# Optimization experiments

Measured on AMD Instinct MI355X. Metric: run time of the kernel, lower is better.

## Reference

```python
import jax, jax.numpy as jnp
import numpy as np

B, L, C, H, RATIO = 2, 512, 256, 8, 4
D = C // H
EPS = 1e-5


def layernorm(x, g, b):
    m = jnp.mean(x, axis=-1, keepdims=True)
    v = jnp.mean((x - m) ** 2, axis=-1, keepdims=True)
    return (x - m) * jax.lax.rsqrt(v + EPS) * g + b


def setup_inputs() -> dict:
    key = jax.random.key(0)
    ks = jax.random.split(key, 10)
    s = 0.02
    return {
        "x": jax.random.normal(ks[0], (B, L, C), jnp.float32),
        "relative_pos": jax.random.normal(ks[1], (B, L, L, C), jnp.float32),
        # attention params (qkv_bias=False)
        "w_qkv": jax.random.normal(ks[2], (C, 3 * C), jnp.float32) * s,
        "w_proj": jax.random.normal(ks[3], (C, C), jnp.float32) * s,
        "b_proj": jnp.zeros((C,), jnp.float32),
        # relative_project: Linear(C,H) -> GELU -> LayerNorm(H)
        "w_rel": jax.random.normal(ks[4], (C, H), jnp.float32) * s,
        "b_rel": jnp.zeros((H,), jnp.float32),
        "g_reln": jnp.ones((H,), jnp.float32),
        "b_reln": jnp.zeros((H,), jnp.float32),
        # block layernorms
        "g_n1": jnp.ones((C,), jnp.float32),
        "b_n1": jnp.zeros((C,), jnp.float32),
        "g_n2": jnp.ones((C,), jnp.float32),
        "b_n2": jnp.zeros((C,), jnp.float32),
        # MLP (mlp_ratio=4, act=GELU)
        "w_mlp1": jax.random.normal(ks[5], (C, RATIO * C), jnp.float32) * s,
        "b_mlp1": jnp.zeros((RATIO * C,), jnp.float32),
        "w_mlp2": jax.random.normal(ks[6], (RATIO * C, C), jnp.float32) * s,
        "b_mlp2": jnp.zeros((C,), jnp.float32),
    }


def reference(x, relative_pos, w_qkv, w_proj, b_proj, w_rel, b_rel,
              g_reln, b_reln, g_n1, b_n1, g_n2, b_n2,
              w_mlp1, b_mlp1, w_mlp2, b_mlp2):
    # eval mode: dropout / droppath are identity
    scale = D ** -0.5

    # --- attention branch ---
    h = layernorm(x, g_n1, b_n1)                      # [B,L,C]
    qkv = (h @ w_qkv).reshape(B, L, 3, H, D)
    qkv = jnp.transpose(qkv, (2, 0, 3, 1, 4))          # [3,B,H,L,D]
    q, k, v = qkv[0], qkv[1], qkv[2]

    attn = jnp.einsum("bhid,bhjd->bhij", q, k)        # [B,H,L,L]

    # relative bias: Linear -> GELU(exact) -> LayerNorm over heads
    rel = jax.nn.gelu(relative_pos @ w_rel + b_rel, approximate=False)  # [B,L,L,H]
    rel = layernorm(rel, g_reln, b_reln)
    rel = jnp.transpose(rel, (0, 3, 1, 2))            # [B,H,L,L]

    attn = jax.nn.softmax((attn + rel) * scale, axis=-1)
    o = jnp.einsum("bhij,bhjd->bhid", attn, v)        # [B,H,L,D]
    o = jnp.transpose(o, (0, 2, 1, 3)).reshape(B, L, C)
    o = o @ w_proj + b_proj
    x = x + o

    # --- MLP branch (jump=False since out_feat==in_feat) ---
    h = layernorm(x, g_n2, b_n2)
    h = jax.nn.gelu(h @ w_mlp1 + b_mlp1, approximate=False)
    h = h @ w_mlp2 + b_mlp2
    return x + h
```

## Files before the change

### kernel.cpp

```cpp
#include <hip/hip_runtime.h>
#include <hip/hip_bf16.h>
#include <cstddef>

#define EPS_ 1e-5f
#define SCALE_ 0.1767766952966369f

typedef short bf16x8_t __attribute__((ext_vector_type(8)));
typedef float f32x4_t  __attribute__((ext_vector_type(4)));

__device__ __forceinline__ float gelu_f(float x) {
    float y = 0.7978845608028654f * (x + 0.044715f * x * x * x);
    float e = __expf(2.0f * y);
    float t = 1.0f - 2.0f * __builtin_amdgcn_rcpf(e + 1.0f);
    return 0.5f * x * (1.0f + t);
}
__device__ __forceinline__ unsigned short f2bf(float f) {
    return __builtin_bit_cast(unsigned short, __float2bfloat16(f));
}
__device__ __forceinline__ unsigned f2bf2(float a, float b) {
    unsigned lo = __builtin_bit_cast(unsigned short, __float2bfloat16(a));
    unsigned hi = __builtin_bit_cast(unsigned short, __float2bfloat16(b));
    return lo | (hi << 16);
}
__device__ __forceinline__ float bf2f(unsigned short s) {
    unsigned u = (unsigned)s << 16;
    return __builtin_bit_cast(float, u);
}

__global__ __launch_bounds__(256) void ln_kernel(const float* __restrict__ x,
                                                 const float* __restrict__ g,
                                                 const float* __restrict__ b,
                                                 unsigned short* __restrict__ out) {
    int wid = threadIdx.x >> 6, lane = threadIdx.x & 63;
    int row = blockIdx.x * 4 + wid;
    const float4 xv = *(const float4*)(x + (size_t)row * 256 + lane * 4);
    float s  = xv.x + xv.y + xv.z + xv.w;
    float sq = xv.x*xv.x + xv.y*xv.y + xv.z*xv.z + xv.w*xv.w;
#pragma unroll
    for (int m = 1; m < 64; m <<= 1) { s += __shfl_xor(s, m); sq += __shfl_xor(sq, m); }
    float mean = s * (1.0f/256.0f);
    float var  = sq * (1.0f/256.0f) - mean*mean;
    float rstd = rsqrtf(var + EPS_);
    float4 gv = *(const float4*)(g + lane*4);
    float4 bv = *(const float4*)(b + lane*4);
    uint2 o;
    o.x = f2bf2((xv.x-mean)*rstd*gv.x + bv.x, (xv.y-mean)*rstd*gv.y + bv.y);
    o.y = f2bf2((xv.z-mean)*rstd*gv.z + bv.z, (xv.w-mean)*rstd*gv.w + bv.w);
    *(uint2*)(out + (size_t)row * 256 + lane * 4) = o;
}

__global__ __launch_bounds__(256) void convw_kernel(
    const float* __restrict__ w_qkv,  unsigned short* __restrict__ wqkvT,
    const float* __restrict__ w_proj, unsigned short* __restrict__ wprojT,
    const float* __restrict__ w_mlp1, unsigned short* __restrict__ wmlp1T,
    const float* __restrict__ w_mlp2, unsigned short* __restrict__ wmlp2T) {
    __shared__ float tile[32][33];
    int bid = blockIdx.x, t = threadIdx.x;
    const float* W; unsigned short* WT; int K, N, tt;
    if (bid < 192)      { W = w_qkv;  WT = wqkvT;  K = 256;  N = 768;  tt = bid; }
    else if (bid < 256) { W = w_proj; WT = wprojT; K = 256;  N = 256;  tt = bid - 192; }
    else if (bid < 512) { W = w_mlp1; WT = wmlp1T; K = 256;  N = 1024; tt = bid - 256; }
    else                { W = w_mlp2; WT = wmlp2T; K = 1024; N = 256;  tt = bid - 512; }
    int ntn = N >> 5;
    int kt = tt / ntn, nt = tt % ntn;
    int k0 = kt * 32, n0 = nt * 32;
    {
        int kr = t >> 3, cg = (t & 7) * 4;
        float4 v = *(const float4*)(W + (size_t)(k0 + kr) * N + n0 + cg);
        tile[kr][cg+0] = v.x; tile[kr][cg+1] = v.y; tile[kr][cg+2] = v.z; tile[kr][cg+3] = v.w;
    }
    __syncthreads();
    {
        int nr = t >> 3, kg = (t & 7) * 4;
        uint2 o;
        o.x = f2bf2(tile[kg+0][nr], tile[kg+1][nr]);
        o.y = f2bf2(tile[kg+2][nr], tile[kg+3][nr]);
        *(uint2*)(WT + (size_t)(n0 + nr) * K + k0 + kg) = o;
    }
}

template<bool BIAS, bool GACT, bool RESID, bool BF16OUT, int KSPLIT>
__global__ __launch_bounds__(256) void mgemm_kernel(
    const unsigned short* __restrict__ A, const unsigned short* __restrict__ BT,
    const float* __restrict__ bias, const float* __restrict__ resid,
    void* __restrict__ Cout, int M, int N, int K) {
    __shared__ unsigned short Al[64][40];
    __shared__ unsigned short Bl[64][40];
    int t = threadIdx.x;
    int bm = blockIdx.x, bn = blockIdx.y, kz = blockIdx.z;
    int kchunk = K / KSPLIT;
    int srow = t >> 2, skk = (t & 3) * 8;
    const unsigned short* Ap = A  + (size_t)(bm*64 + srow) * K + kz*kchunk + skk;
    const unsigned short* Bp = BT + (size_t)(bn*64 + srow) * K + kz*kchunk + skk;
    int lane = t & 63, w = t >> 6, wr = w >> 1, wc = w & 1;
    int fr = lane & 15, fg = lane >> 4;
    f32x4_t a00 = {0.f,0.f,0.f,0.f}, a01 = {0.f,0.f,0.f,0.f};
    f32x4_t a10 = {0.f,0.f,0.f,0.f}, a11 = {0.f,0.f,0.f,0.f};
    for (int kk = 0; kk < kchunk; kk += 32) {
        uint4 av = *(const uint4*)(Ap + kk);
        uint4 bv = *(const uint4*)(Bp + kk);
        __syncthreads();
        *(uint4*)&Al[srow][skk] = av;
        *(uint4*)&Bl[srow][skk] = bv;
        __syncthreads();
        bf16x8_t fa0 = *(const bf16x8_t*)&Al[wr*32      + fr][fg*8];
        bf16x8_t fa1 = *(const bf16x8_t*)&Al[wr*32 + 16 + fr][fg*8];
        bf16x8_t fb0 = *(const bf16x8_t*)&Bl[wc*32      + fr][fg*8];
        bf16x8_t fb1 = *(const bf16x8_t*)&Bl[wc*32 + 16 + fr][fg*8];
        a00 = __builtin_amdgcn_mfma_f32_16x16x32_bf16(fa0, fb0, a00, 0, 0, 0);
        a01 = __builtin_amdgcn_mfma_f32_16x16x32_bf16(fa0, fb1, a01, 0, 0, 0);
        a10 = __builtin_amdgcn_mfma_f32_16x16x32_bf16(fa1, fb0, a10, 0, 0, 0);
        a11 = __builtin_amdgcn_mfma_f32_16x16x32_bf16(fa1, fb1, a11, 0, 0, 0);
    }
    float* Cf = (float*)Cout + (KSPLIT > 1 ? (size_t)kz * M * N : (size_t)0);
    unsigned short* Cb = (unsigned short*)Cout;
    auto emit = [&](f32x4_t acc, int mi, int ni) {
        int Ro = bm*64 + wr*32 + mi*16 + fg*4;
        int Co = bn*64 + wc*32 + ni*16 + fr;
        float bval = BIAS ? bias[Co] : 0.f;
#pragma unroll
        for (int e = 0; e < 4; ++e) {
            int r = Ro + e;
            float v = acc[e];
            if (BIAS)  v += bval;
            if (GACT)  v = gelu_f(v);
            if (RESID) v += resid[(size_t)r * N + Co];
            if (BF16OUT) Cb[(size_t)r * N + Co] = f2bf(v);
            else         Cf[(size_t)r * N + Co] = v;
        }
    };
    emit(a00, 0, 0); emit(a01, 0, 1); emit(a10, 1, 0); emit(a11, 1, 1);
}

__global__ __launch_bounds__(256) void qk_kernel(const float* __restrict__ qkv,
                                                 float* __restrict__ qk) {
    __shared__ float k_lds[512*32];
    int t = threadIdx.x;
    int it = blockIdx.x;
    int h  = blockIdx.y;
    int b  = blockIdx.z;
    const float* base = qkv + (size_t)b * 393216;
#pragma unroll
    for (int r = 0; r < 16; ++r) {
        int idx = r*256 + t;
        int row = idx >> 3, c4 = idx & 7;
        float4 kv = *(const float4*)(base + (size_t)row*768 + 256 + h*32 + c4*4);
        *(float4*)(k_lds + row*32 + c4*4) = kv;
    }
    __syncthreads();
    int ir = t & 31, jg = t >> 5;
    int i = it*32 + ir;
    float4 q[8];
    const float* qp = base + (size_t)i*768 + h*32;
#pragma unroll
    for (int c4 = 0; c4 < 8; ++c4) q[c4] = *(const float4*)(qp + c4*4);
    float* outp = qk + (((size_t)(b*512 + i))*8 + h)*512 + jg*64;
    for (int jj = 0; jj < 64; jj += 4) {
        float a4[4];
#pragma unroll
        for (int u = 0; u < 4; ++u) {
            const float* kp = k_lds + (size_t)(jg*64 + jj + u)*32;
            float acc = 0.f;
#pragma unroll
            for (int c4 = 0; c4 < 8; ++c4) {
                float4 kv = *(const float4*)(kp + c4*4);
                acc += q[c4].x*kv.x + q[c4].y*kv.y + q[c4].z*kv.z + q[c4].w*kv.w;
            }
            a4[u] = acc;
        }
        *(float4*)(outp + jj) = make_float4(a4[0], a4[1], a4[2], a4[3]);
    }
}

#define LGS 520
__global__ __launch_bounds__(256) void rel_softmax_kernel(
    const float* __restrict__ rp, const float* __restrict__ qk,
    const float* __restrict__ w_rel, const float* __restrict__ b_rel,
    const float* __restrict__ g_reln, const float* __restrict__ b_reln,
    unsigned short* __restrict__ attn) {
    __shared__ float lg_lds[8*LGS];
    int t = threadIdx.x;
    int bi = blockIdx.x;
    int wid = t >> 6, lane = t & 63;
    int fr = lane & 15, fg = lane >> 4;
    bool act = fr < 8;
    bf16x8_t bfrag[8];
#pragma unroll
    for (int kk = 0; kk < 8; ++kk) {
        bf16x8_t bf;
#pragma unroll
        for (int e = 0; e < 8; ++e) {
            float v = act ? w_rel[(size_t)(kk*32 + fg*8 + e)*8 + fr] : 0.f;
            bf[e] = (short)f2bf(v);
        }
        bfrag[kk] = bf;
    }
    float brel = act ? b_rel[fr]  : 0.f;
    float grn  = act ? g_reln[fr] : 1.f;
    float brn  = act ? b_reln[fr] : 0.f;
    const float* rpb = rp + (size_t)bi * 512 * 256;
#pragma unroll 1
    for (int tile = 0; tile < 8; ++tile) {
        int j0 = wid*128 + tile*16;
        const float* arow = rpb + (size_t)(j0 + fr)*256 + fg*8;
        f32x4_t acc = {0.f,0.f,0.f,0.f};
#pragma unroll
        for (int kk = 0; kk < 8; ++kk) {
            float4 x0 = *(const float4*)(arow + kk*32);
            float4 x1 = *(const float4*)(arow + kk*32 + 4);
            union { bf16x8_t v; uint4 u; } cvt;
            cvt.u.x = f2bf2(x0.x, x0.y);
            cvt.u.y = f2bf2(x0.z, x0.w);
            cvt.u.z = f2bf2(x1.x, x1.y);
            cvt.u.w = f2bf2(x1.z, x1.w);
            acc = __builtin_amdgcn_mfma_f32_16x16x32_bf16(cvt.v, bfrag[kk], acc, 0, 0, 0);
        }
#pragma unroll
        for (int r = 0; r < 4; ++r) {
            float val = acc[r] + brel;
            float gv = gelu_f(val);
            float sm = gv, sq = gv*gv;
            sm += __shfl_xor(sm, 1); sq += __shfl_xor(sq, 1);
            sm += __shfl_xor(sm, 2); sq += __shfl_xor(sq, 2);
            sm += __shfl_xor(sm, 4); sq += __shfl_xor(sq, 4);
            float mean = sm * 0.125f;
            float var  = sq * 0.125f - mean*mean;
            float reln = (gv - mean) * rsqrtf(var + EPS_) * grn + brn;
            if (act) lg_lds[fr*LGS + j0 + fg*4 + r] = reln;
        }
    }
    __syncthreads();
    {
        int h = wid*2 + (lane >> 5);
        int sub = lane & 31;
        const float* row  = lg_lds + h*LGS;
        const float* qrow = qk + ((size_t)bi*8 + h)*512;
        float v[16];
#pragma unroll
        for (int c4 = 0; c4 < 4; ++c4) {
            float4 r4 = *(const float4*)(row  + c4*128 + sub*4);
            float4 q4 = *(const float4*)(qrow + c4*128 + sub*4);
            v[c4*4+0] = (q4.x + r4.x) * SCALE_;
            v[c4*4+1] = (q4.y + r4.y) * SCALE_;
            v[c4*4+2] = (q4.z + r4.z) * SCALE_;
            v[c4*4+3] = (q4.w + r4.w) * SCALE_;
        }
        float mx = v[0];
#pragma unroll
        for (int e = 1; e < 16; ++e) mx = fmaxf(mx, v[e]);
#pragma unroll
        for (int m = 1; m < 32; m <<= 1) mx = fmaxf(mx, __shfl_xor(mx, m));
        float s = 0.f;
#pragma unroll
        for (int e = 0; e < 16; ++e) { v[e] = __expf(v[e] - mx); s += v[e]; }
#pragma unroll
        for (int m = 1; m < 32; m <<= 1) s += __shfl_xor(s, m);
        float inv = 1.0f / s;
#pragma unroll
        for (int e = 0; e < 16; ++e) v[e] *= inv;
        unsigned short* dst = attn + (size_t)bi*4096 + h*512;
#pragma unroll
        for (int c4 = 0; c4 < 4; ++c4) {
            uint2 o2;
            o2.x = f2bf2(v[c4*4+0], v[c4*4+1]);
            o2.y = f2bf2(v[c4*4+2], v[c4*4+3]);
            *(uint2*)(dst + c4*128 + sub*4) = o2;
        }
    }
}

__global__ __launch_bounds__(256) void attnv_kernel(const unsigned short* __restrict__ attn,
                                                    const float* __restrict__ qkv,
                                                    unsigned short* __restrict__ o) {
    __shared__ float a_lds[4*8*512];
    int t = threadIdx.x;
    int bi0 = blockIdx.x * 4;
    int b = bi0 >> 9;
    const ushort4* asrc = (const ushort4*)(attn + (size_t)bi0*4096);
#pragma unroll
    for (int r = 0; r < 16; ++r) {
        ushort4 s4 = asrc[r*256 + t];
        float4 f4 = make_float4(bf2f(s4.x), bf2f(s4.y), bf2f(s4.z), bf2f(s4.w));
        *(float4*)(a_lds + (size_t)(r*256 + t)*4) = f4;
    }
    __syncthreads();
    int c = t, h = c >> 5;
    const float* vcol = qkv + (size_t)b*393216 + 512 + c;
    float acc0 = 0.f, acc1 = 0.f, acc2 = 0.f, acc3 = 0.f;
    for (int j = 0; j < 512; j += 2) {
        float vv0 = vcol[(size_t)j*768];
        float vv1 = vcol[(size_t)(j+1)*768];
        acc0 += a_lds[(0*8+h)*512 + j]*vv0 + a_lds[(0*8+h)*512 + j+1]*vv1;
        acc1 += a_lds[(1*8+h)*512 + j]*vv0 + a_lds[(1*8+h)*512 + j+1]*vv1;
        acc2 += a_lds[(2*8+h)*512 + j]*vv0 + a_lds[(2*8+h)*512 + j+1]*vv1;
        acc3 += a_lds[(3*8+h)*512 + j]*vv0 + a_lds[(3*8+h)*512 + j+1]*vv1;
    }
    o[(size_t)(bi0+0)*256 + c] = f2bf(acc0);
    o[(size_t)(bi0+1)*256 + c] = f2bf(acc1);
    o[(size_t)(bi0+2)*256 + c] = f2bf(acc2);
    o[(size_t)(bi0+3)*256 + c] = f2bf(acc3);
}

__global__ __launch_bounds__(256) void combine_kernel(const float* __restrict__ part,
                                                      const float* __restrict__ bias,
                                                      const float* __restrict__ resid,
                                                      float* __restrict__ out) {
    int f = blockIdx.x * 256 + threadIdx.x;
    int e = f * 4;
    float4 r  = *(const float4*)(resid + e);
    float4 bv = *(const float4*)(bias + (e & 255));
    float4 p0 = *(const float4*)(part + e);
    float4 p1 = *(const float4*)(part + 262144 + e);
    float4 p2 = *(const float4*)(part + 524288 + e);
    float4 p3 = *(const float4*)(part + 786432 + e);
    float4 o4;
    o4.x = r.x + bv.x + p0.x + p1.x + p2.x + p3.x;
    o4.y = r.y + bv.y + p0.y + p1.y + p2.y + p3.y;
    o4.z = r.z + bv.z + p0.z + p1.z + p2.z + p3.z;
    o4.w = r.w + bv.w + p0.w + p1.w + p2.w + p3.w;
    *(float4*)(out + e) = o4;
}

extern "C" void kernel_launch(void* const* d_in, const int* in_sizes, int n_in,
                              void* d_out, int out_size, void* d_ws, size_t ws_size,
                              hipStream_t stream) {
    const float* x      = (const float*)d_in[0];
    const float* rp     = (const float*)d_in[1];
    const float* w_qkv  = (const float*)d_in[2];
    const float* w_proj = (const float*)d_in[3];
    const float* b_proj = (const float*)d_in[4];
    const float* w_rel  = (const float*)d_in[5];
    const float* b_rel  = (const float*)d_in[6];
    const float* g_reln = (const float*)d_in[7];
    const float* b_reln = (const float*)d_in[8];
    const float* g_n1   = (const float*)d_in[9];
    const float* b_n1   = (const float*)d_in[10];
    const float* g_n2   = (const float*)d_in[11];
    const float* b_n2   = (const float*)d_in[12];
    const float* w_mlp1 = (const float*)d_in[13];
    const float* b_mlp1 = (const float*)d_in[14];
    const float* w_mlp2 = (const float*)d_in[15];
    const float* b_mlp2 = (const float*)d_in[16];
    float* out = (float*)d_out;

    float* ws      = (float*)d_ws;
    float* ws_qkv  = ws;
    float* ws_qk   = ws_qkv + 786432;
    float* ws_x1   = ws_qk  + 4194304;
    float* ws_pt   = ws_x1  + 262144;
    unsigned short* ub = (unsigned short*)(ws_pt + 1048576);
    unsigned short* attnbf = ub;
    unsigned short* hbf    = attnbf + 4194304;
    unsigned short* obf    = hbf  + 262144;
    unsigned short* h2bf   = obf  + 262144;
    unsigned short* hgbf   = h2bf + 262144;
    unsigned short* wqkvT  = hgbf + 1048576;
    unsigned short* wprojT = wqkvT + 196608;
    unsigned short* wmlp1T = wprojT + 65536;
    unsigned short* wmlp2T = wmlp1T + 262144;

    convw_kernel<<<768, 256, 0, stream>>>(w_qkv, wqkvT, w_proj, wprojT,
                                          w_mlp1, wmlp1T, w_mlp2, wmlp2T);
    ln_kernel<<<256, 256, 0, stream>>>(x, g_n1, b_n1, hbf);
    mgemm_kernel<false,false,false,false,1><<<dim3(16,12,1), 256, 0, stream>>>(
        hbf, wqkvT, nullptr, nullptr, ws_qkv, 1024, 768, 256);
    qk_kernel<<<dim3(16,8,2), 256, 0, stream>>>(ws_qkv, ws_qk);
    rel_softmax_kernel<<<1024, 256, 0, stream>>>(rp, ws_qk, w_rel, b_rel, g_reln, b_reln, attnbf);
    attnv_kernel<<<256, 256, 0, stream>>>(attnbf, ws_qkv, obf);
    mgemm_kernel<true,false,true,false,1><<<dim3(16,4,1), 256, 0, stream>>>(
        obf, wprojT, b_proj, x, ws_x1, 1024, 256, 256);
    ln_kernel<<<256, 256, 0, stream>>>(ws_x1, g_n2, b_n2, h2bf);
    mgemm_kernel<true,true,false,true,1><<<dim3(16,16,1), 256, 0, stream>>>(
        h2bf, wmlp1T, b_mlp1, nullptr, hgbf, 1024, 1024, 256);
    mgemm_kernel<false,false,false,false,4><<<dim3(16,4,4), 256, 0, stream>>>(
        hgbf, wmlp2T, nullptr, nullptr, ws_pt, 1024, 256, 1024);
    combine_kernel<<<256, 256, 0, stream>>>(ws_pt, b_mlp2, ws_x1, out);
}
```

Measured before the change: 222.9 us.

## Fuse QK^T into relative-bias softmax kernel and merge LN1 into weight prep

Removes the separate fp32 qk kernel and its 16 MB intermediate buffer. The q·k logits are now computed inside rel_softmax with a bf16 MFMA, using a per-lane selected q fragment so that each head's row block is picked out, and they are added to the relative bias before writing to LDS. The first layernorm is merged into the weight-conversion kernel as extra blocks, saving one launch. The attn·V loop is also widened to float4 LDS reads. The trade-off is that q·k now runs in bf16 instead of fp32, and K is read redundantly from global memory by every row block.

```diff
diff --git a/kernel.cpp b/kernel.cpp
--- a/kernel.cpp
+++ b/kernel.cpp
@@ -27,12 +27,11 @@
     return __builtin_bit_cast(float, u);
 }
 
-__global__ __launch_bounds__(256) void ln_kernel(const float* __restrict__ x,
-                                                 const float* __restrict__ g,
-                                                 const float* __restrict__ b,
-                                                 unsigned short* __restrict__ out) {
-    int wid = threadIdx.x >> 6, lane = threadIdx.x & 63;
-    int row = blockIdx.x * 4 + wid;
+__device__ __forceinline__ void ln_row_body(const float* __restrict__ x,
+                                            const float* __restrict__ g,
+                                            const float* __restrict__ b,
+                                            unsigned short* __restrict__ out,
+                                            int row, int lane) {
     const float4 xv = *(const float4*)(x + (size_t)row * 256 + lane * 4);
     float s  = xv.x + xv.y + xv.z + xv.w;
     float sq = xv.x*xv.x + xv.y*xv.y + xv.z*xv.z + xv.w*xv.w;
@@ -49,13 +48,26 @@
     *(uint2*)(out + (size_t)row * 256 + lane * 4) = o;
 }
 
-__global__ __launch_bounds__(256) void convw_kernel(
+__global__ __launch_bounds__(256) void ln_kernel(const float* __restrict__ x,
+                                                 const float* __restrict__ g,
+                                                 const float* __restrict__ b,
+                                                 unsigned short* __restrict__ out) {
+    ln_row_body(x, g, b, out, blockIdx.x * 4 + (threadIdx.x >> 6), threadIdx.x & 63);
+}
+
+__global__ __launch_bounds__(256) void prep_kernel(
     const float* __restrict__ w_qkv,  unsigned short* __restrict__ wqkvT,
     const float* __restrict__ w_proj, unsigned short* __restrict__ wprojT,
     const float* __restrict__ w_mlp1, unsigned short* __restrict__ wmlp1T,
-    const float* __restrict__ w_mlp2, unsigned short* __restrict__ wmlp2T) {
+    const float* __restrict__ w_mlp2, unsigned short* __restrict__ wmlp2T,
+    const float* __restrict__ x, const float* __restrict__ g_n1,
+    const float* __restrict__ b_n1, unsigned short* __restrict__ hbf) {
     __shared__ float tile[32][33];
     int bid = blockIdx.x, t = threadIdx.x;
+    if (bid >= 768) {
+        ln_row_body(x, g_n1, b_n1, hbf, (bid - 768) * 4 + (t >> 6), t & 63);
+        return;
+    }
     const float* W; unsigned short* WT; int K, N, tt;
     if (bid < 192)      { W = w_qkv;  WT = wqkvT;  K = 256;  N = 768;  tt = bid; }
     else if (bid < 256) { W = w_proj; WT = wprojT; K = 256;  N = 256;  tt = bid - 192; }
@@ -132,55 +144,16 @@
     emit(a00, 0, 0); emit(a01, 0, 1); emit(a10, 1, 0); emit(a11, 1, 1);
 }
 
-__global__ __launch_bounds__(256) void qk_kernel(const float* __restrict__ qkv,
-                                                 float* __restrict__ qk) {
-    __shared__ float k_lds[512*32];
-    int t = threadIdx.x;
-    int it = blockIdx.x;
-    int h  = blockIdx.y;
-    int b  = blockIdx.z;
-    const float* base = qkv + (size_t)b * 393216;
-#pragma unroll
-    for (int r = 0; r < 16; ++r) {
-        int idx = r*256 + t;
-        int row = idx >> 3, c4 = idx & 7;
-        float4 kv = *(const float4*)(base + (size_t)row*768 + 256 + h*32 + c4*4);
-        *(float4*)(k_lds + row*32 + c4*4) = kv;
-    }
-    __syncthreads();
-    int ir = t & 31, jg = t >> 5;
-    int i = it*32 + ir;
-    float4 q[8];
-    const float* qp = base + (size_t)i*768 + h*32;
-#pragma unroll
-    for (int c4 = 0; c4 < 8; ++c4) q[c4] = *(const float4*)(qp + c4*4);
-    float* outp = qk + (((size_t)(b*512 + i))*8 + h)*512 + jg*64;
-    for (int jj = 0; jj < 64; jj += 4) {
-        float a4[4];
-#pragma unroll
-        for (int u = 0; u < 4; ++u) {
-            const float* kp = k_lds + (size_t)(jg*64 + jj + u)*32;
-            float acc = 0.f;
-#pragma unroll
-            for (int c4 = 0; c4 < 8; ++c4) {
-                float4 kv = *(const float4*)(kp + c4*4);
-                acc += q[c4].x*kv.x + q[c4].y*kv.y + q[c4].z*kv.z + q[c4].w*kv.w;
-            }
-            a4[u] = acc;
-        }
-        *(float4*)(outp + jj) = make_float4(a4[0], a4[1], a4[2], a4[3]);
-    }
-}
-
 #define LGS 520
 __global__ __launch_bounds__(256) void rel_softmax_kernel(
-    const float* __restrict__ rp, const float* __restrict__ qk,
+    const float* __restrict__ rp, const float* __restrict__ qkv,
     const float* __restrict__ w_rel, const float* __restrict__ b_rel,
     const float* __restrict__ g_reln, const float* __restrict__ b_reln,
     unsigned short* __restrict__ attn) {
     __shared__ float lg_lds[8*LGS];
     int t = threadIdx.x;
     int bi = blockIdx.x;
+    int b  = bi >> 9;
     int wid = t >> 6, lane = t & 63;
     int fr = lane & 15, fg = lane >> 4;
     bool act = fr < 8;
@@ -195,29 +168,48 @@
         }
         bfrag[kk] = bf;
     }
+    bf16x8_t bqk; bf16x8_t bz;
+#pragma unroll
+    for (int e = 0; e < 8; ++e) { bqk[e] = 0; bz[e] = 0; }
+    if (act) {
+        const float* qp = qkv + (size_t)bi * 768 + fr*32 + fg*8;
+        float4 q0 = *(const float4*)(qp);
+        float4 q1 = *(const float4*)(qp + 4);
+        union { bf16x8_t v; uint4 u; } cq;
+        cq.u.x = f2bf2(q0.x, q0.y); cq.u.y = f2bf2(q0.z, q0.w);
+        cq.u.z = f2bf2(q1.x, q1.y); cq.u.w = f2bf2(q1.z, q1.w);
+        bqk = cq.v;
+    }
     float brel = act ? b_rel[fr]  : 0.f;
     float grn  = act ? g_reln[fr] : 1.f;
     float brn  = act ? b_reln[fr] : 0.f;
     const float* rpb = rp + (size_t)bi * 512 * 256;
+    const float* kb  = qkv + (size_t)b * 393216 + 256;
 #pragma unroll 1
     for (int tile = 0; tile < 8; ++tile) {
         int j0 = wid*128 + tile*16;
         const float* arow = rpb + (size_t)(j0 + fr)*256 + fg*8;
-        f32x4_t acc = {0.f,0.f,0.f,0.f};
+        const float* krow = kb  + (size_t)(j0 + fr)*768 + fg*8;
+        f32x4_t accR = {0.f,0.f,0.f,0.f};
+        f32x4_t accQ = {0.f,0.f,0.f,0.f};
 #pragma unroll
         for (int kk = 0; kk < 8; ++kk) {
             float4 x0 = *(const float4*)(arow + kk*32);
             float4 x1 = *(const float4*)(arow + kk*32 + 4);
-            union { bf16x8_t v; uint4 u; } cvt;
-            cvt.u.x = f2bf2(x0.x, x0.y);
-            cvt.u.y = f2bf2(x0.z, x0.w);
-            cvt.u.z = f2bf2(x1.x, x1.y);
-            cvt.u.w = f2bf2(x1.z, x1.w);
-            acc = __builtin_amdgcn_mfma_f32_16x16x32_bf16(cvt.v, bfrag[kk], acc, 0, 0, 0);
+            float4 y0 = *(const float4*)(krow + kk*32);
+            float4 y1 = *(const float4*)(krow + kk*32 + 4);
+            union { bf16x8_t v; uint4 u; } ca, ck;
+            ca.u.x = f2bf2(x0.x, x0.y); ca.u.y = f2bf2(x0.z, x0.w);
+            ca.u.z = f2bf2(x1.x, x1.y); ca.u.w = f2bf2(x1.z, x1.w);
+            ck.u.x = f2bf2(y0.x, y0.y); ck.u.y = f2bf2(y0.z, y0.w);
+            ck.u.z = f2bf2(y1.x, y1.y); ck.u.w = f2bf2(y1.z, y1.w);
+            accR = __builtin_amdgcn_mfma_f32_16x16x32_bf16(ca.v, bfrag[kk], accR, 0, 0, 0);
+            bf16x8_t bsel = (fr == kk) ? bqk : bz;
+            accQ = __builtin_amdgcn_mfma_f32_16x16x32_bf16(ck.v, bsel, accQ, 0, 0, 0);
         }
 #pragma unroll
         for (int r = 0; r < 4; ++r) {
-            float val = acc[r] + brel;
+            float val = accR[r] + brel;
             float gv = gelu_f(val);
             float sm = gv, sq = gv*gv;
             sm += __shfl_xor(sm, 1); sq += __shfl_xor(sq, 1);
@@ -226,24 +218,20 @@
             float mean = sm * 0.125f;
             float var  = sq * 0.125f - mean*mean;
             float reln = (gv - mean) * rsqrtf(var + EPS_) * grn + brn;
-            if (act) lg_lds[fr*LGS + j0 + fg*4 + r] = reln;
+            float lg = (reln + accQ[r]) * SCALE_;
+            if (act) lg_lds[fr*LGS + j0 + fg*4 + r] = lg;
         }
     }
     __syncthreads();
     {
         int h = wid*2 + (lane >> 5);
         int sub = lane & 31;
-        const float* row  = lg_lds + h*LGS;
-        const float* qrow = qk + ((size_t)bi*8 + h)*512;
+        const float* row = lg_lds + h*LGS;
         float v[16];
 #pragma unroll
         for (int c4 = 0; c4 < 4; ++c4) {
-            float4 r4 = *(const float4*)(row  + c4*128 + sub*4);
-            float4 q4 = *(const float4*)(qrow + c4*128 + sub*4);
-            v[c4*4+0] = (q4.x + r4.x) * SCALE_;
-            v[c4*4+1] = (q4.y + r4.y) * SCALE_;
-            v[c4*4+2] = (q4.z + r4.z) * SCALE_;
-            v[c4*4+3] = (q4.w + r4.w) * SCALE_;
+            float4 r4 = *(const float4*)(row + c4*128 + sub*4);
+            v[c4*4+0] = r4.x; v[c4*4+1] = r4.y; v[c4*4+2] = r4.z; v[c4*4+3] = r4.w;
         }
         float mx = v[0];
 #pragma unroll
@@ -287,13 +275,19 @@
     int c = t, h = c >> 5;
     const float* vcol = qkv + (size_t)b*393216 + 512 + c;
     float acc0 = 0.f, acc1 = 0.f, acc2 = 0.f, acc3 = 0.f;
-    for (int j = 0; j < 512; j += 2) {
-        float vv0 = vcol[(size_t)j*768];
+    for (int j = 0; j < 512; j += 4) {
+        float vv0 = vcol[(size_t)(j+0)*768];
         float vv1 = vcol[(size_t)(j+1)*768];
-        acc0 += a_lds[(0*8+h)*512 + j]*vv0 + a_lds[(0*8+h)*512 + j+1]*vv1;
-        acc1 += a_lds[(1*8+h)*512 + j]*vv0 + a_lds[(1*8+h)*512 + j+1]*vv1;
-        acc2 += a_lds[(2*8+h)*512 + j]*vv0 + a_lds[(2*8+h)*512 + j+1]*vv1;
-        acc3 += a_lds[(3*8+h)*512 + j]*vv0 + a_lds[(3*8+h)*512 + j+1]*vv1;
+        float vv2 = vcol[(size_t)(j+2)*768];
+        float vv3 = vcol[(size_t)(j+3)*768];
+        float4 a0 = *(const float4*)(a_lds + (0*8+h)*512 + j);
+        float4 a1 = *(const float4*)(a_lds + (1*8+h)*512 + j);
+        float4 a2 = *(const float4*)(a_lds + (2*8+h)*512 + j);
+        float4 a3 = *(const float4*)(a_lds + (3*8+h)*512 + j);
+        acc0 += a0.x*vv0 + a0.y*vv1 + a0.z*vv2 + a0.w*vv3;
+        acc1 += a1.x*vv0 + a1.y*vv1 + a1.z*vv2 + a1.w*vv3;
+        acc2 += a2.x*vv0 + a2.y*vv1 + a2.z*vv2 + a2.w*vv3;
+        acc3 += a3.x*vv0 + a3.y*vv1 + a3.z*vv2 + a3.w*vv3;
     }
     o[(size_t)(bi0+0)*256 + c] = f2bf(acc0);
     o[(size_t)(bi0+1)*256 + c] = f2bf(acc1);
@@ -345,8 +339,7 @@
 
     float* ws      = (float*)d_ws;
     float* ws_qkv  = ws;
-    float* ws_qk   = ws_qkv + 786432;
-    float* ws_x1   = ws_qk  + 4194304;
+    float* ws_x1   = ws_qkv + 786432;
     float* ws_pt   = ws_x1  + 262144;
     unsigned short* ub = (unsigned short*)(ws_pt + 1048576);
     unsigned short* attnbf = ub;
@@ -359,13 +352,12 @@
     unsigned short* wmlp1T = wprojT + 65536;
     unsigned short* wmlp2T = wmlp1T + 262144;
 
-    convw_kernel<<<768, 256, 0, stream>>>(w_qkv, wqkvT, w_proj, wprojT,
-                                          w_mlp1, wmlp1T, w_mlp2, wmlp2T);
-    ln_kernel<<<256, 256, 0, stream>>>(x, g_n1, b_n1, hbf);
+    prep_kernel<<<1024, 256, 0, stream>>>(w_qkv, wqkvT, w_proj, wprojT,
+                                          w_mlp1, wmlp1T, w_mlp2, wmlp2T,
+                                          x, g_n1, b_n1, hbf);
     mgemm_kernel<false,false,false,false,1><<<dim3(16,12,1), 256, 0, stream>>>(
         hbf, wqkvT, nullptr, nullptr, ws_qkv, 1024, 768, 256);
-    qk_kernel<<<dim3(16,8,2), 256, 0, stream>>>(ws_qkv, ws_qk);
-    rel_softmax_kernel<<<1024, 256, 0, stream>>>(rp, ws_qk, w_rel, b_rel, g_reln, b_reln, attnbf);
+    rel_softmax_kernel<<<1024, 256, 0, stream>>>(rp, ws_qkv, w_rel, b_rel, g_reln, b_reln, attnbf);
     attnv_kernel<<<256, 256, 0, stream>>>(attnbf, ws_qkv, obf);
     mgemm_kernel<true,false,true,false,1><<<dim3(16,4,1), 256, 0, stream>>>(
         obf, wprojT, b_proj, x, ws_x1, 1024, 256, 256);
```

After: 238.4 us. 7.0% more time.

## Fuse rel-softmax, attn@V, output projection and LN2 into one kernel

Applied to the files above, without the earlier changes.

Merges the relative-bias softmax, the attention-times-V product, the output projection with bias and residual, and the second layernorm into one per-row kernel. This removes the bf16 attention round trip through global memory and three launches. The LN1 computation is also folded into the weight-conversion prep kernel. The projection now runs as a scalar fp32 loop over global w_proj per row instead of an MFMA GEMM, which adds per-block global reads of the projection weights and V columns.

```diff
diff --git a/kernel.cpp b/kernel.cpp
--- a/kernel.cpp
+++ b/kernel.cpp
@@ -22,17 +22,12 @@
     unsigned hi = __builtin_bit_cast(unsigned short, __float2bfloat16(b));
     return lo | (hi << 16);
 }
-__device__ __forceinline__ float bf2f(unsigned short s) {
-    unsigned u = (unsigned)s << 16;
-    return __builtin_bit_cast(float, u);
-}
-
-__global__ __launch_bounds__(256) void ln_kernel(const float* __restrict__ x,
-                                                 const float* __restrict__ g,
-                                                 const float* __restrict__ b,
-                                                 unsigned short* __restrict__ out) {
-    int wid = threadIdx.x >> 6, lane = threadIdx.x & 63;
-    int row = blockIdx.x * 4 + wid;
+
+__device__ __forceinline__ void ln_row_body(const float* __restrict__ x,
+                                            const float* __restrict__ g,
+                                            const float* __restrict__ b,
+                                            unsigned short* __restrict__ out,
+                                            int row, int lane) {
     const float4 xv = *(const float4*)(x + (size_t)row * 256 + lane * 4);
     float s  = xv.x + xv.y + xv.z + xv.w;
     float sq = xv.x*xv.x + xv.y*xv.y + xv.z*xv.z + xv.w*xv.w;
@@ -49,18 +44,22 @@
     *(uint2*)(out + (size_t)row * 256 + lane * 4) = o;
 }
 
-__global__ __launch_bounds__(256) void convw_kernel(
+__global__ __launch_bounds__(256) void prep_kernel(
     const float* __restrict__ w_qkv,  unsigned short* __restrict__ wqkvT,
-    const float* __restrict__ w_proj, unsigned short* __restrict__ wprojT,
     const float* __restrict__ w_mlp1, unsigned short* __restrict__ wmlp1T,
-    const float* __restrict__ w_mlp2, unsigned short* __restrict__ wmlp2T) {
+    const float* __restrict__ w_mlp2, unsigned short* __restrict__ wmlp2T,
+    const float* __restrict__ x, const float* __restrict__ g_n1,
+    const float* __restrict__ b_n1, unsigned short* __restrict__ hbf) {
     __shared__ float tile[32][33];
     int bid = blockIdx.x, t = threadIdx.x;
+    if (bid >= 704) {
+        ln_row_body(x, g_n1, b_n1, hbf, (bid - 704) * 4 + (t >> 6), t & 63);
+        return;
+    }
     const float* W; unsigned short* WT; int K, N, tt;
     if (bid < 192)      { W = w_qkv;  WT = wqkvT;  K = 256;  N = 768;  tt = bid; }
-    else if (bid < 256) { W = w_proj; WT = wprojT; K = 256;  N = 256;  tt = bid - 192; }
-    else if (bid < 512) { W = w_mlp1; WT = wmlp1T; K = 256;  N = 1024; tt = bid - 256; }
-    else                { W = w_mlp2; WT = wmlp2T; K = 1024; N = 256;  tt = bid - 512; }
+    else if (bid < 448) { W = w_mlp1; WT = wmlp1T; K = 256;  N = 1024; tt = bid - 192; }
+    else                { W = w_mlp2; WT = wmlp2T; K = 1024; N = 256;  tt = bid - 448; }
     int ntn = N >> 5;
     int kt = tt / ntn, nt = tt % ntn;
     int k0 = kt * 32, n0 = nt * 32;
@@ -79,10 +78,10 @@
     }
 }
 
-template<bool BIAS, bool GACT, bool RESID, bool BF16OUT, int KSPLIT>
+template<bool BIAS, bool GACT, bool BF16OUT, int KSPLIT>
 __global__ __launch_bounds__(256) void mgemm_kernel(
     const unsigned short* __restrict__ A, const unsigned short* __restrict__ BT,
-    const float* __restrict__ bias, const float* __restrict__ resid,
+    const float* __restrict__ bias,
     void* __restrict__ Cout, int M, int N, int K) {
     __shared__ unsigned short Al[64][40];
     __shared__ unsigned short Bl[64][40];
@@ -124,7 +123,6 @@
             float v = acc[e];
             if (BIAS)  v += bval;
             if (GACT)  v = gelu_f(v);
-            if (RESID) v += resid[(size_t)r * N + Co];
             if (BF16OUT) Cb[(size_t)r * N + Co] = f2bf(v);
             else         Cf[(size_t)r * N + Co] = v;
         }
@@ -173,14 +171,21 @@
 }
 
 #define LGS 520
-__global__ __launch_bounds__(256) void rel_softmax_kernel(
+__global__ __launch_bounds__(256) void rel_mega_kernel(
     const float* __restrict__ rp, const float* __restrict__ qk,
+    const float* __restrict__ qkv,
     const float* __restrict__ w_rel, const float* __restrict__ b_rel,
     const float* __restrict__ g_reln, const float* __restrict__ b_reln,
-    unsigned short* __restrict__ attn) {
+    const float* __restrict__ w_proj, const float* __restrict__ b_proj,
+    const float* __restrict__ x, const float* __restrict__ g_n2,
+    const float* __restrict__ b_n2,
+    float* __restrict__ x1_out, unsigned short* __restrict__ h2bf) {
     __shared__ float lg_lds[8*LGS];
+    __shared__ float o_lds[256];
+    __shared__ float red[8];
     int t = threadIdx.x;
     int bi = blockIdx.x;
+    int b  = bi >> 9;
     int wid = t >> 6, lane = t & 63;
     int fr = lane & 15, fg = lane >> 4;
     bool act = fr < 8;
@@ -233,7 +238,7 @@
     {
         int h = wid*2 + (lane >> 5);
         int sub = lane & 31;
-        const float* row  = lg_lds + h*LGS;
+        float* row = lg_lds + h*LGS;
         const float* qrow = qk + ((size_t)bi*8 + h)*512;
         float v[16];
 #pragma unroll
@@ -258,47 +263,55 @@
         float inv = 1.0f / s;
 #pragma unroll
         for (int e = 0; e < 16; ++e) v[e] *= inv;
-        unsigned short* dst = attn + (size_t)bi*4096 + h*512;
 #pragma unroll
         for (int c4 = 0; c4 < 4; ++c4) {
-            uint2 o2;
-            o2.x = f2bf2(v[c4*4+0], v[c4*4+1]);
-            o2.y = f2bf2(v[c4*4+2], v[c4*4+3]);
-            *(uint2*)(dst + c4*128 + sub*4) = o2;
-        }
-    }
-}
-
-__global__ __launch_bounds__(256) void attnv_kernel(const unsigned short* __restrict__ attn,
-                                                    const float* __restrict__ qkv,
-                                                    unsigned short* __restrict__ o) {
-    __shared__ float a_lds[4*8*512];
-    int t = threadIdx.x;
-    int bi0 = blockIdx.x * 4;
-    int b = bi0 >> 9;
-    const ushort4* asrc = (const ushort4*)(attn + (size_t)bi0*4096);
-#pragma unroll
-    for (int r = 0; r < 16; ++r) {
-        ushort4 s4 = asrc[r*256 + t];
-        float4 f4 = make_float4(bf2f(s4.x), bf2f(s4.y), bf2f(s4.z), bf2f(s4.w));
-        *(float4*)(a_lds + (size_t)(r*256 + t)*4) = f4;
-    }
-    __syncthreads();
-    int c = t, h = c >> 5;
-    const float* vcol = qkv + (size_t)b*393216 + 512 + c;
-    float acc0 = 0.f, acc1 = 0.f, acc2 = 0.f, acc3 = 0.f;
-    for (int j = 0; j < 512; j += 2) {
-        float vv0 = vcol[(size_t)j*768];
-        float vv1 = vcol[(size_t)(j+1)*768];
-        acc0 += a_lds[(0*8+h)*512 + j]*vv0 + a_lds[(0*8+h)*512 + j+1]*vv1;
-        acc1 += a_lds[(1*8+h)*512 + j]*vv0 + a_lds[(1*8+h)*512 + j+1]*vv1;
-        acc2 += a_lds[(2*8+h)*512 + j]*vv0 + a_lds[(2*8+h)*512 + j+1]*vv1;
-        acc3 += a_lds[(3*8+h)*512 + j]*vv0 + a_lds[(3*8+h)*512 + j+1]*vv1;
-    }
-    o[(size_t)(bi0+0)*256 + c] = f2bf(acc0);
-    o[(size_t)(bi0+1)*256 + c] = f2bf(acc1);
-    o[(size_t)(bi0+2)*256 + c] = f2bf(acc2);
-    o[(size_t)(bi0+3)*256 + c] = f2bf(acc3);
+            float4 o4 = make_float4(v[c4*4+0], v[c4*4+1], v[c4*4+2], v[c4*4+3]);
+            *(float4*)(row + c4*128 + sub*4) = o4;
+        }
+    }
+    __syncthreads();
+    {
+        int c = t, h = c >> 5;
+        const float* vcol = qkv + (size_t)b*393216 + 512 + c;
+        const float* arow = lg_lds + h*LGS;
+        float acc = 0.f;
+        for (int j = 0; j < 512; j += 4) {
+            float4 a4 = *(const float4*)(arow + j);
+            acc += a4.x * vcol[(size_t)(j+0)*768];
+            acc += a4.y * vcol[(size_t)(j+1)*768];
+            acc += a4.z * vcol[(size_t)(j+2)*768];
+            acc += a4.w * vcol[(size_t)(j+3)*768];
+        }
+        o_lds[c] = acc;
+    }
+    __syncthreads();
+    float x1c;
+    {
+        int c = t;
+        float acc2 = 0.f;
+        for (int k = 0; k < 256; k += 4) {
+            acc2 += o_lds[k+0] * w_proj[(size_t)(k+0)*256 + c];
+            acc2 += o_lds[k+1] * w_proj[(size_t)(k+1)*256 + c];
+            acc2 += o_lds[k+2] * w_proj[(size_t)(k+2)*256 + c];
+            acc2 += o_lds[k+3] * w_proj[(size_t)(k+3)*256 + c];
+        }
+        x1c = x[(size_t)bi*256 + c] + b_proj[c] + acc2;
+        x1_out[(size_t)bi*256 + c] = x1c;
+    }
+    {
+        float s = x1c, sq = x1c*x1c;
+#pragma unroll
+        for (int m = 1; m < 64; m <<= 1) { s += __shfl_xor(s, m); sq += __shfl_xor(sq, m); }
+        if (lane == 0) { red[wid*2] = s; red[wid*2+1] = sq; }
+        __syncthreads();
+        float S  = red[0] + red[2] + red[4] + red[6];
+        float SQ = red[1] + red[3] + red[5] + red[7];
+        float mean = S * (1.0f/256.0f);
+        float var  = SQ * (1.0f/256.0f) - mean*mean;
+        float rstd = rsqrtf(var + EPS_);
+        float h2 = (x1c - mean) * rstd * g_n2[t] + b_n2[t];
+        h2bf[(size_t)bi*256 + t] = f2bf(h2);
+    }
 }
 
 __global__ __launch_bounds__(256) void combine_kernel(const float* __restrict__ part,
@@ -349,30 +362,24 @@
     float* ws_x1   = ws_qk  + 4194304;
     float* ws_pt   = ws_x1  + 262144;
     unsigned short* ub = (unsigned short*)(ws_pt + 1048576);
-    unsigned short* attnbf = ub;
-    unsigned short* hbf    = attnbf + 4194304;
-    unsigned short* obf    = hbf  + 262144;
-    unsigned short* h2bf   = obf  + 262144;
+    unsigned short* hbf    = ub;
+    unsigned short* h2bf   = hbf  + 262144;
     unsigned short* hgbf   = h2bf + 262144;
     unsigned short* wqkvT  = hgbf + 1048576;
-    unsigned short* wprojT = wqkvT + 196608;
-    unsigned short* wmlp1T = wprojT + 65536;
+    unsigned short* wmlp1T = wqkvT + 196608;
     unsigned short* wmlp2T = wmlp1T + 262144;
 
-    convw_kernel<<<768, 256, 0, stream>>>(w_qkv, wqkvT, w_proj, wprojT,
-                                          w_mlp1, wmlp1T, w_mlp2, wmlp2T);
-    ln_kernel<<<256, 256, 0, stream>>>(x, g_n1, b_n1, hbf);
-    mgemm_kernel<false,false,false,false,1><<<dim3(16,12,1), 256, 0, stream>>>(
-        hbf, wqkvT, nullptr, nullptr, ws_qkv, 1024, 768, 256);
+    prep_kernel<<<960, 256, 0, stream>>>(w_qkv, wqkvT, w_mlp1, wmlp1T, w_mlp2, wmlp2T,
+                                         x, g_n1, b_n1, hbf);
+    mgemm_kernel<false,false,false,1><<<dim3(16,12,1), 256, 0, stream>>>(
+        hbf, wqkvT, nullptr, ws_qkv, 1024, 768, 256);
     qk_kernel<<<dim3(16,8,2), 256, 0, stream>>>(ws_qkv, ws_qk);
-    rel_softmax_kernel<<<1024, 256, 0, stream>>>(rp, ws_qk, w_rel, b_rel, g_reln, b_reln, attnbf);
-    attnv_kernel<<<256, 256, 0, stream>>>(attnbf, ws_qkv, obf);
-    mgemm_kernel<true,false,true,false,1><<<dim3(16,4,1), 256, 0, stream>>>(
-        obf, wprojT, b_proj, x, ws_x1, 1024, 256, 256);
-    ln_kernel<<<256, 256, 0, stream>>>(ws_x1, g_n2, b_n2, h2bf);
-    mgemm_kernel<true,true,false,true,1><<<dim3(16,16,1), 256, 0, stream>>>(
-        h2bf, wmlp1T, b_mlp1, nullptr, hgbf, 1024, 1024, 256);
-    mgemm_kernel<false,false,false,false,4><<<dim3(16,4,4), 256, 0, stream>>>(
-        hgbf, wmlp2T, nullptr, nullptr, ws_pt, 1024, 256, 1024);
+    rel_mega_kernel<<<1024, 256, 0, stream>>>(rp, ws_qk, ws_qkv, w_rel, b_rel,
+                                              g_reln, b_reln, w_proj, b_proj,
+                                              x, g_n2, b_n2, ws_x1, h2bf);
+    mgemm_kernel<true,true,true,1><<<dim3(16,16,1), 256, 0, stream>>>(
+        h2bf, wmlp1T, b_mlp1, hgbf, 1024, 1024, 256);
+    mgemm_kernel<false,false,false,4><<<dim3(16,4,4), 256, 0, stream>>>(
+        hgbf, wmlp2T, nullptr, ws_pt, 1024, 256, 1024);
     combine_kernel<<<256, 256, 0, stream>>>(ws_pt, b_mlp2, ws_x1, out);
 }
```

New measurement: 200.5 us. 10.0% less time.
